# Optimization experiments

Measured on AMD Instinct MI355X. Metric: run time of the kernel, lower is better.

Reference implementation:

```python
import jax, jax.numpy as jnp
from jax import lax
import numpy as np

HID = 32

def setup_inputs() -> dict:
    key = jax.random.key(0)
    ks = jax.random.split(key, 8)
    B, T = 4096, 1024
    x = jax.random.normal(ks[0], (B, T, 1), dtype=jnp.float32)
    h = jnp.zeros((1, B, HID), dtype=jnp.float32)
    s = 1.0 / np.sqrt(HID)  # PyTorch GRU init scale
    W_ih = jax.random.uniform(ks[1], (3 * HID, 1), minval=-s, maxval=s, dtype=jnp.float32)
    W_hh = jax.random.uniform(ks[2], (3 * HID, HID), minval=-s, maxval=s, dtype=jnp.float32)
    b_ih = jax.random.uniform(ks[3], (3 * HID,), minval=-s, maxval=s, dtype=jnp.float32)
    b_hh = jax.random.uniform(ks[4], (3 * HID,), minval=-s, maxval=s, dtype=jnp.float32)
    W_out = jax.random.uniform(ks[5], (1, HID), minval=-s, maxval=s, dtype=jnp.float32)
    b_out = jax.random.uniform(ks[6], (1,), minval=-s, maxval=s, dtype=jnp.float32)
    return {"x": x, "h": h, "W_ih": W_ih, "W_hh": W_hh, "b_ih": b_ih,
            "b_hh": b_hh, "W_out": W_out, "b_out": b_out}

def _gru(x, h0, W_ih, W_hh, b_ih, b_hh):
    # Precompute input projections for all timesteps: [B, T, 3H]
    xi = jnp.einsum('bti,gi->btg', x, W_ih) + b_ih

    def step(h, xi_t):
        gh = h @ W_hh.T + b_hh                      # [B, 3H]
        ir, iz, inn = jnp.split(xi_t, 3, axis=-1)
        hr, hz, hn = jnp.split(gh, 3, axis=-1)
        r = jax.nn.sigmoid(ir + hr)
        z = jax.nn.sigmoid(iz + hz)
        n = jnp.tanh(inn + r * hn)
        h_new = (1.0 - z) * n + z * h               # PyTorch GRU update
        return h_new, h_new

    h_last, hs = lax.scan(step, h0, jnp.swapaxes(xi, 0, 1))  # time-major scan
    return jnp.swapaxes(hs, 0, 1), h_last            # [B,T,H], [B,H]

def reference(x, h, W_ih, W_hh, b_ih, b_hh, W_out, b_out):
    h0 = h[0]                                        # [B, H]
    seq, h_last = _gru(x, h0, W_ih, W_hh, b_ih, b_hh)
    out = jnp.einsum('bth,oh->bto', seq, W_out) + b_out  # [B, T, 1]
    return out, h_last[None]                         # h: [1, B, H]
```

## Files before the change

kernel.cpp:

```cpp
#include <hip/hip_runtime.h>
#include <hip/hip_bf16.h>

#define BATCH 4096
#define T_LEN 1024
#define HID 32
#define CT 64
#define NCHUNK (T_LEN / CT)
#define L2E 1.4426950408889634f

typedef short bf16x8 __attribute__((ext_vector_type(8)));
typedef float f32x4 __attribute__((ext_vector_type(4)));

__device__ __forceinline__ short bf16hi_rne(float f, float* back) {
    unsigned u = __float_as_uint(f);
    unsigned r = (u + 0x7fffu + ((u >> 16) & 1u)) & 0xffff0000u;
    *back = __uint_as_float(r);
    return (short)(r >> 16);
}
__device__ __forceinline__ float fast_rcp(float x)  { return __builtin_amdgcn_rcpf(x); }
__device__ __forceinline__ float fast_exp2(float x) { return __builtin_amdgcn_exp2f(x); }

__global__ void __launch_bounds__(128, 1)
gru_fused3(const float* __restrict__ xg, const float* __restrict__ h0g,
           const float* __restrict__ Wih, const float* __restrict__ Whh,
           const float* __restrict__ bih, const float* __restrict__ bhh,
           const float* __restrict__ Wout, const float* __restrict__ boutp,
           float* __restrict__ outp)
{
    const int tid = threadIdx.x;
    const int w   = tid >> 6;
    const int l   = tid & 63;
    const int rg  = (l >> 4) & 3;
    const int cl  = l & 15;
    const int b0  = blockIdx.x << 4;

    __shared__ float xbuf[16][68];
    __shared__ float po[8][16][68];
    __shared__ __align__(16) short exch[2][2][64 * 8];

    bf16x8 WAhi[3], WAlo[3];
#pragma unroll
    for (int q = 0; q < 3; ++q) {
        const int m = 2 * q + w;
        const float sc = (q < 2) ? L2E : 2.0f * L2E;
#pragma unroll
        for (int i = 0; i < 8; ++i) {
            int j = 16 * ((i >> 2) ^ w) + 4 * rg + (i & 3);
            float wv = Whh[(m * 16 + cl) * HID + j] * sc;
            float hf, d;
            WAhi[q][i] = bf16hi_rne(wv, &hf);
            WAlo[q][i] = bf16hi_rne(wv - hf, &d);
        }
    }
    float wrz[8], brz[8], win[4], bin[4], wout4[4];
    f32x4 biasN;
#pragma unroll
    for (int q = 0; q < 2; ++q)
#pragma unroll
        for (int r = 0; r < 4; ++r) {
            int g = (2 * q + w) * 16 + 4 * rg + r;
            wrz[q * 4 + r] = L2E * Wih[g];
            brz[q * 4 + r] = L2E * (bih[g] + bhh[g]);
        }
#pragma unroll
    for (int r = 0; r < 4; ++r) {
        int g = (4 + w) * 16 + 4 * rg + r;
        win[r]   = 2.0f * L2E * Wih[g];
        bin[r]   = 2.0f * L2E * bih[g];
        biasN[r] = 2.0f * L2E * bhh[g];
        wout4[r] = Wout[16 * w + 4 * rg + r];
    }
    const float bout = boutp[0];

    float h[4];
    bf16x8 Bhi, Blo;
#pragma unroll
    for (int i = 0; i < 8; ++i) {
        int j = 16 * ((i >> 2) ^ w) + 4 * rg + (i & 3);
        float hv = h0g[(size_t)(b0 + cl) * HID + j];
        float hf, d;
        Bhi[i] = bf16hi_rne(hv, &hf);
        Blo[i] = bf16hi_rne(hv - hf, &d);
    }
#pragma unroll
    for (int r = 0; r < 4; ++r)
        h[r] = h0g[(size_t)(b0 + cl) * HID + 16 * w + 4 * rg + r];

    short* const exMy       = &exch[0][w][l * 8];
    const short* const exOt = &exch[0][1 - w][l * 8];

    for (int tc = 0; tc < NCHUNK; ++tc) {
        if (tc > 0) {
            int row = tid >> 3, t0 = (tid & 7) * 8;
            f32x4 s0 = {bout, bout, bout, bout}, s1 = s0;
#pragma unroll
            for (int g = 0; g < 8; ++g) {
                s0 += *reinterpret_cast<const f32x4*>(&po[g][row][t0]);
                s1 += *reinterpret_cast<const f32x4*>(&po[g][row][t0 + 4]);
            }
            float* dst = &outp[(size_t)(b0 + row) * T_LEN + (tc - 1) * CT + t0];
            *reinterpret_cast<f32x4*>(dst)     = s0;
            *reinterpret_cast<f32x4*>(dst + 4) = s1;
        }
#pragma unroll
        for (int q = 0; q < 8; ++q)
            xbuf[w * 8 + q][l] = xg[(size_t)(b0 + w * 8 + q) * T_LEN + tc * CT + l];
        __syncthreads();
        f32x4 xq = *reinterpret_cast<const f32x4*>(&xbuf[cl][0]);

        for (int qt = 0; qt < 16; ++qt) {
            f32x4 xqn = *reinterpret_cast<const f32x4*>(&xbuf[cl][((qt + 1) & 15) * 4]);
            f32x4 opv;
#pragma unroll
            for (int s = 0; s < 4; ++s) {
                const float xv = xq[s];
                f32x4 i0, i1;
#pragma unroll
                for (int r = 0; r < 4; ++r) {
                    i0[r] = fmaf(xv, wrz[r],     brz[r]);
                    i1[r] = fmaf(xv, wrz[4 + r], brz[4 + r]);
                }
                f32x4 a0 = __builtin_amdgcn_mfma_f32_16x16x32_bf16(WAhi[0], Bhi, i0,    0, 0, 0);
                f32x4 a1 = __builtin_amdgcn_mfma_f32_16x16x32_bf16(WAhi[1], Bhi, i1,    0, 0, 0);
                f32x4 a2 = __builtin_amdgcn_mfma_f32_16x16x32_bf16(WAhi[2], Bhi, biasN, 0, 0, 0);
                a0 = __builtin_amdgcn_mfma_f32_16x16x32_bf16(WAhi[0], Blo, a0, 0, 0, 0);
                a1 = __builtin_amdgcn_mfma_f32_16x16x32_bf16(WAhi[1], Blo, a1, 0, 0, 0);
                a2 = __builtin_amdgcn_mfma_f32_16x16x32_bf16(WAhi[2], Blo, a2, 0, 0, 0);
                a0 = __builtin_amdgcn_mfma_f32_16x16x32_bf16(WAlo[0], Bhi, a0, 0, 0, 0);
                a1 = __builtin_amdgcn_mfma_f32_16x16x32_bf16(WAlo[1], Bhi, a1, 0, 0, 0);
                a2 = __builtin_amdgcn_mfma_f32_16x16x32_bf16(WAlo[2], Bhi, a2, 0, 0, 0);

                bf16x8 pk;
                float op = 0.f;
#pragma unroll
                for (int r = 0; r < 4; ++r) {
                    float rr = fast_rcp(1.f + fast_exp2(-a0[r]));
                    float zz = fast_rcp(1.f + fast_exp2(-a1[r]));
                    float np = fmaf(rr, a2[r], fmaf(xv, win[r], bin[r]));
                    float nn = fmaf(-2.f, fast_rcp(1.f + fast_exp2(np)), 1.f);
                    float hv = fmaf(zz, h[r] - nn, nn);
                    h[r] = hv;
                    op = fmaf(hv, wout4[r], op);
                    float hf;
                    pk[r]     = bf16hi_rne(hv, &hf);
                    pk[4 + r] = (short)(__float_as_uint(hv - hf) >> 16);
                }
                opv[s] = op;
                *reinterpret_cast<bf16x8*>(exMy + (s & 1) * 1024) = pk;
                if (s == 3)
                    *reinterpret_cast<f32x4*>(&po[w * 4 + rg][cl][qt * 4]) = opv;
                __syncthreads();
                bf16x8 oth = *reinterpret_cast<const bf16x8*>(exOt + (s & 1) * 1024);
#pragma unroll
                for (int r = 0; r < 4; ++r) {
                    Bhi[r]     = pk[r];      Blo[r]     = pk[4 + r];
                    Bhi[4 + r] = oth[r];     Blo[4 + r] = oth[4 + r];
                }
            }
            xq = xqn;
        }
    }

    {
        int row = tid >> 3, t0 = (tid & 7) * 8;
        f32x4 s0 = {bout, bout, bout, bout}, s1 = s0;
#pragma unroll
        for (int g = 0; g < 8; ++g) {
            s0 += *reinterpret_cast<const f32x4*>(&po[g][row][t0]);
            s1 += *reinterpret_cast<const f32x4*>(&po[g][row][t0 + 4]);
        }
        float* dst = &outp[(size_t)(b0 + row) * T_LEN + (NCHUNK - 1) * CT + t0];
        *reinterpret_cast<f32x4*>(dst)     = s0;
        *reinterpret_cast<f32x4*>(dst + 4) = s1;
    }

#pragma unroll
    for (int r = 0; r < 4; ++r)
        outp[(size_t)BATCH * T_LEN + (size_t)(b0 + cl) * HID + 16 * w + 4 * rg + r] = h[r];
}

extern "C" void kernel_launch(void* const* d_in, const int* in_sizes, int n_in,
                              void* d_out, int out_size, void* d_ws, size_t ws_size,
                              hipStream_t stream) {
    const float* x     = (const float*)d_in[0];
    const float* h0    = (const float*)d_in[1];
    const float* Wih   = (const float*)d_in[2];
    const float* Whh   = (const float*)d_in[3];
    const float* bihv  = (const float*)d_in[4];
    const float* bhhv  = (const float*)d_in[5];
    const float* Woutv = (const float*)d_in[6];
    const float* boutv = (const float*)d_in[7];
    float* out = (float*)d_out;

    gru_fused3<<<dim3(BATCH / 16), dim3(128), 0, stream>>>(
        x, h0, Wih, Whh, bihv, bhhv, Woutv, boutv, out);
}
```

Baseline: 460.1 us.

## Split recurrent MFMA into own-half and exchanged-half products to overlap LDS exchange

```diff
diff --git a/kernel.cpp b/kernel.cpp
--- a/kernel.cpp
+++ b/kernel.cpp
@@ -20,8 +20,10 @@
 __device__ __forceinline__ float fast_rcp(float x)  { return __builtin_amdgcn_rcpf(x); }
 __device__ __forceinline__ float fast_exp2(float x) { return __builtin_amdgcn_exp2f(x); }
 
+#define MFMA __builtin_amdgcn_mfma_f32_16x16x32_bf16
+
 __global__ void __launch_bounds__(128, 1)
-gru_fused3(const float* __restrict__ xg, const float* __restrict__ h0g,
+gru_fused5(const float* __restrict__ xg, const float* __restrict__ h0g,
            const float* __restrict__ Wih, const float* __restrict__ Whh,
            const float* __restrict__ bih, const float* __restrict__ bhh,
            const float* __restrict__ Wout, const float* __restrict__ boutp,
@@ -38,22 +40,29 @@
     __shared__ float po[8][16][68];
     __shared__ __align__(16) short exch[2][2][64 * 8];
 
-    bf16x8 WAhi[3], WAlo[3];
+    bf16x8 AownHi[3], AownLo[3], AothHi[3], AothLo[3];
 #pragma unroll
     for (int q = 0; q < 3; ++q) {
         const int m = 2 * q + w;
         const float sc = (q < 2) ? L2E : 2.0f * L2E;
 #pragma unroll
         for (int i = 0; i < 8; ++i) {
-            int j = 16 * ((i >> 2) ^ w) + 4 * rg + (i & 3);
-            float wv = Whh[(m * 16 + cl) * HID + j] * sc;
-            float hf, d;
-            WAhi[q][i] = bf16hi_rne(wv, &hf);
-            WAlo[q][i] = bf16hi_rne(wv - hf, &d);
+            if (i < 4) {
+                float hf, d;
+                float wv = Whh[(m * 16 + cl) * HID + 16 * w + 4 * rg + i] * sc;
+                AownHi[q][i] = bf16hi_rne(wv, &hf);
+                AownLo[q][i] = bf16hi_rne(wv - hf, &d);
+                float wv2 = Whh[(m * 16 + cl) * HID + 16 * (1 - w) + 4 * rg + i] * sc;
+                AothHi[q][i] = bf16hi_rne(wv2, &hf);
+                AothLo[q][i] = bf16hi_rne(wv2 - hf, &d);
+            } else {
+                AownHi[q][i] = 0; AownLo[q][i] = 0;
+                AothHi[q][i] = 0; AothLo[q][i] = 0;
+            }
         }
     }
     float wrz[8], brz[8], win[4], bin[4], wout4[4];
-    f32x4 biasN;
+    f32x4 bN;
 #pragma unroll
     for (int q = 0; q < 2; ++q)
 #pragma unroll
@@ -67,24 +76,24 @@
         int g = (4 + w) * 16 + 4 * rg + r;
         win[r]   = 2.0f * L2E * Wih[g];
         bin[r]   = 2.0f * L2E * bih[g];
-        biasN[r] = 2.0f * L2E * bhh[g];
+        bN[r]    = 2.0f * L2E * bhh[g];
         wout4[r] = Wout[16 * w + 4 * rg + r];
     }
     const float bout = boutp[0];
 
     float h[4];
-    bf16x8 Bhi, Blo;
-#pragma unroll
-    for (int i = 0; i < 8; ++i) {
-        int j = 16 * ((i >> 2) ^ w) + 4 * rg + (i & 3);
-        float hv = h0g[(size_t)(b0 + cl) * HID + j];
-        float hf, d;
-        Bhi[i] = bf16hi_rne(hv, &hf);
-        Blo[i] = bf16hi_rne(hv - hf, &d);
-    }
-#pragma unroll
-    for (int r = 0; r < 4; ++r)
-        h[r] = h0g[(size_t)(b0 + cl) * HID + 16 * w + 4 * rg + r];
+    bf16x8 pk, R;
+#pragma unroll
+    for (int r = 0; r < 4; ++r) {
+        float hv = h0g[(size_t)(b0 + cl) * HID + 16 * w + 4 * rg + r];
+        h[r] = hv;
+        float hf;
+        pk[r]     = bf16hi_rne(hv, &hf);
+        pk[4 + r] = (short)(__float_as_uint(hv - hf) >> 16);
+        float ov = h0g[(size_t)(b0 + cl) * HID + 16 * (1 - w) + 4 * rg + r];
+        R[r]     = bf16hi_rne(ov, &hf);
+        R[4 + r] = (short)(__float_as_uint(ov - hf) >> 16);
+    }
 
     short* const exMy       = &exch[0][w][l * 8];
     const short* const exOt = &exch[0][1 - w][l * 8];
@@ -114,48 +123,56 @@
 #pragma unroll
             for (int s = 0; s < 4; ++s) {
                 const float xv = xq[s];
-                f32x4 i0, i1;
+                bf16x8 pkLo = __builtin_shufflevector(pk, pk, 4, 5, 6, 7, 0, 1, 2, 3);
+                bf16x8 RLo  = __builtin_shufflevector(R,  R,  4, 5, 6, 7, 0, 1, 2, 3);
+                f32x4 iR, iZ;
 #pragma unroll
                 for (int r = 0; r < 4; ++r) {
-                    i0[r] = fmaf(xv, wrz[r],     brz[r]);
-                    i1[r] = fmaf(xv, wrz[4 + r], brz[4 + r]);
+                    iR[r] = fmaf(xv, wrz[r],     brz[r]);
+                    iZ[r] = fmaf(xv, wrz[4 + r], brz[4 + r]);
                 }
-                f32x4 a0 = __builtin_amdgcn_mfma_f32_16x16x32_bf16(WAhi[0], Bhi, i0,    0, 0, 0);
-                f32x4 a1 = __builtin_amdgcn_mfma_f32_16x16x32_bf16(WAhi[1], Bhi, i1,    0, 0, 0);
-                f32x4 a2 = __builtin_amdgcn_mfma_f32_16x16x32_bf16(WAhi[2], Bhi, biasN, 0, 0, 0);
-                a0 = __builtin_amdgcn_mfma_f32_16x16x32_bf16(WAhi[0], Blo, a0, 0, 0, 0);
-                a1 = __builtin_amdgcn_mfma_f32_16x16x32_bf16(WAhi[1], Blo, a1, 0, 0, 0);
-                a2 = __builtin_amdgcn_mfma_f32_16x16x32_bf16(WAhi[2], Blo, a2, 0, 0, 0);
-                a0 = __builtin_amdgcn_mfma_f32_16x16x32_bf16(WAlo[0], Bhi, a0, 0, 0, 0);
-                a1 = __builtin_amdgcn_mfma_f32_16x16x32_bf16(WAlo[1], Bhi, a1, 0, 0, 0);
-                a2 = __builtin_amdgcn_mfma_f32_16x16x32_bf16(WAlo[2], Bhi, a2, 0, 0, 0);
-
-                bf16x8 pk;
+                f32x4 aR, aZ, aN;
+                aR = MFMA(AownHi[0], pk,   iR, 0, 0, 0);
+                aZ = MFMA(AownHi[1], pk,   iZ, 0, 0, 0);
+                aN = MFMA(AownHi[2], pk,   bN, 0, 0, 0);
+                aR = MFMA(AownLo[0], pk,   aR, 0, 0, 0);
+                aZ = MFMA(AownLo[1], pk,   aZ, 0, 0, 0);
+                aN = MFMA(AownLo[2], pk,   aN, 0, 0, 0);
+                aR = MFMA(AownHi[0], pkLo, aR, 0, 0, 0);
+                aZ = MFMA(AownHi[1], pkLo, aZ, 0, 0, 0);
+                aN = MFMA(AownHi[2], pkLo, aN, 0, 0, 0);
+                aR = MFMA(AothHi[0], R,    aR, 0, 0, 0);
+                aZ = MFMA(AothHi[1], R,    aZ, 0, 0, 0);
+                aN = MFMA(AothHi[2], R,    aN, 0, 0, 0);
+                aR = MFMA(AothLo[0], R,    aR, 0, 0, 0);
+                aZ = MFMA(AothLo[1], R,    aZ, 0, 0, 0);
+                aN = MFMA(AothLo[2], R,    aN, 0, 0, 0);
+                aR = MFMA(AothHi[0], RLo,  aR, 0, 0, 0);
+                aZ = MFMA(AothHi[1], RLo,  aZ, 0, 0, 0);
+                aN = MFMA(AothHi[2], RLo,  aN, 0, 0, 0);
+
+                bf16x8 npk;
                 float op = 0.f;
 #pragma unroll
                 for (int r = 0; r < 4; ++r) {
-                    float rr = fast_rcp(1.f + fast_exp2(-a0[r]));
-                    float zz = fast_rcp(1.f + fast_exp2(-a1[r]));
-                    float np = fmaf(rr, a2[r], fmaf(xv, win[r], bin[r]));
+                    float rr = fast_rcp(1.f + fast_exp2(-aR[r]));
+                    float zz = fast_rcp(1.f + fast_exp2(-aZ[r]));
+                    float np = fmaf(rr, aN[r], fmaf(xv, win[r], bin[r]));
                     float nn = fmaf(-2.f, fast_rcp(1.f + fast_exp2(np)), 1.f);
                     float hv = fmaf(zz, h[r] - nn, nn);
                     h[r] = hv;
                     op = fmaf(hv, wout4[r], op);
                     float hf;
-                    pk[r]     = bf16hi_rne(hv, &hf);
-                    pk[4 + r] = (short)(__float_as_uint(hv - hf) >> 16);
+                    npk[r]     = bf16hi_rne(hv, &hf);
+                    npk[4 + r] = (short)(__float_as_uint(hv - hf) >> 16);
                 }
+                pk = npk;
                 opv[s] = op;
                 *reinterpret_cast<bf16x8*>(exMy + (s & 1) * 1024) = pk;
                 if (s == 3)
                     *reinterpret_cast<f32x4*>(&po[w * 4 + rg][cl][qt * 4]) = opv;
                 __syncthreads();
-                bf16x8 oth = *reinterpret_cast<const bf16x8*>(exOt + (s & 1) * 1024);
-#pragma unroll
-                for (int r = 0; r < 4; ++r) {
-                    Bhi[r]     = pk[r];      Blo[r]     = pk[4 + r];
-                    Bhi[4 + r] = oth[r];     Blo[4 + r] = oth[4 + r];
-                }
+                R = *reinterpret_cast<const bf16x8*>(exOt + (s & 1) * 1024);
             }
             xq = xqn;
         }
@@ -192,6 +209,6 @@
     const float* boutv = (const float*)d_in[7];
     float* out = (float*)d_out;
 
-    gru_fused3<<<dim3(BATCH / 16), dim3(128), 0, stream>>>(
+    gru_fused5<<<dim3(BATCH / 16), dim3(128), 0, stream>>>(
         x, h0, Wih, Whh, bihv, bhhv, Woutv, boutv, out);
 }
```

Result: slower. 491.5 us (+6.8%).

## Split GRU hidden units across four waves with duplicated-A bf16 split MFMA layout

Applied to the files above, without the earlier changes.

```diff
diff --git a/kernel.cpp b/kernel.cpp
--- a/kernel.cpp
+++ b/kernel.cpp
@@ -9,6 +9,7 @@
 #define L2E 1.4426950408889634f
 
 typedef short bf16x8 __attribute__((ext_vector_type(8)));
+typedef short short4v __attribute__((ext_vector_type(4)));
 typedef float f32x4 __attribute__((ext_vector_type(4)));
 
 __device__ __forceinline__ short bf16hi_rne(float f, float* back) {
@@ -20,91 +21,110 @@
 __device__ __forceinline__ float fast_rcp(float x)  { return __builtin_amdgcn_rcpf(x); }
 __device__ __forceinline__ float fast_exp2(float x) { return __builtin_amdgcn_exp2f(x); }
 
-__global__ void __launch_bounds__(128, 1)
-gru_fused3(const float* __restrict__ xg, const float* __restrict__ h0g,
+#define MFMA __builtin_amdgcn_mfma_f32_16x16x32_bf16
+
+__global__ void __launch_bounds__(256, 1)
+gru_fused6(const float* __restrict__ xg, const float* __restrict__ h0g,
            const float* __restrict__ Wih, const float* __restrict__ Whh,
            const float* __restrict__ bih, const float* __restrict__ bhh,
            const float* __restrict__ Wout, const float* __restrict__ boutp,
            float* __restrict__ outp)
 {
-    const int tid = threadIdx.x;
-    const int w   = tid >> 6;
-    const int l   = tid & 63;
-    const int rg  = (l >> 4) & 3;
-    const int cl  = l & 15;
-    const int b0  = blockIdx.x << 4;
+    const int tid  = threadIdx.x;
+    const int v    = tid >> 6;
+    const int half = v & 1;
+    const int sub  = v >> 1;
+    const int l    = tid & 63;
+    const int rg   = (l >> 4) & 3;
+    const int cl   = l & 15;
+    const int b0   = blockIdx.x << 4;
 
     __shared__ float xbuf[16][68];
-    __shared__ float po[8][16][68];
-    __shared__ __align__(16) short exch[2][2][64 * 8];
-
-    bf16x8 WAhi[3], WAlo[3];
+    __shared__ float po[16][16][68];
+    __shared__ __align__(16) short ex[2][2][4][16][8];
+    const int PAR = 2 * 4 * 16 * 8;
+
+    bf16x8 A1[3][2], A2[3][2];
+    const int phicl = 4 * (cl >> 2) + 2 * sub + (cl & 1);
 #pragma unroll
     for (int q = 0; q < 3; ++q) {
-        const int m = 2 * q + w;
+        const int m = 2 * q + half;
         const float sc = (q < 2) ? L2E : 2.0f * L2E;
-#pragma unroll
-        for (int i = 0; i < 8; ++i) {
-            int j = 16 * ((i >> 2) ^ w) + 4 * rg + (i & 3);
-            float wv = Whh[(m * 16 + cl) * HID + j] * sc;
-            float hf, d;
-            WAhi[q][i] = bf16hi_rne(wv, &hf);
-            WAlo[q][i] = bf16hi_rne(wv - hf, &d);
-        }
-    }
-    float wrz[8], brz[8], win[4], bin[4], wout4[4];
-    f32x4 biasN;
-#pragma unroll
-    for (int q = 0; q < 2; ++q)
-#pragma unroll
-        for (int r = 0; r < 4; ++r) {
-            int g = (2 * q + w) * 16 + 4 * rg + r;
-            wrz[q * 4 + r] = L2E * Wih[g];
-            brz[q * 4 + r] = L2E * (bih[g] + bhh[g]);
-        }
-#pragma unroll
-    for (int r = 0; r < 4; ++r) {
-        int g = (4 + w) * 16 + 4 * rg + r;
-        win[r]   = 2.0f * L2E * Wih[g];
-        bin[r]   = 2.0f * L2E * bih[g];
-        biasN[r] = 2.0f * L2E * bhh[g];
-        wout4[r] = Wout[16 * w + 4 * rg + r];
+        const int grow = m * 16 + phicl;
+#pragma unroll
+        for (int kh = 0; kh < 2; ++kh)
+#pragma unroll
+            for (int qs = 0; qs < 4; ++qs) {
+                float wv = Whh[grow * HID + 16 * kh + 4 * rg + qs] * sc;
+                float hf, d;
+                short hi = bf16hi_rne(wv, &hf);
+                short lo = bf16hi_rne(wv - hf, &d);
+                int shi = (qs < 2) ? qs : qs + 2;
+                int slo = (qs < 2) ? qs + 2 : qs + 4;
+                A1[q][kh][shi] = hi;  A1[q][kh][slo] = hi;
+                A2[q][kh][shi] = lo;  A2[q][kh][slo] = 0;
+            }
+    }
+    float wr4[4], br4[4], wz4[4], bz4[4], wn2[2], bn2[2], wo2[2];
+    f32x4 bN;
+#pragma unroll
+    for (int u = 0; u < 4; ++u) {
+        int rrow = 4 * rg + 2 * sub + (u & 1);
+        int gr = half * 16 + rrow;
+        int gz = (2 + half) * 16 + rrow;
+        int gn = (4 + half) * 16 + rrow;
+        wr4[u] = L2E * Wih[gr];  br4[u] = L2E * (bih[gr] + bhh[gr]);
+        wz4[u] = L2E * Wih[gz];  bz4[u] = L2E * (bih[gz] + bhh[gz]);
+        bN[u]  = 2.0f * L2E * bhh[gn];
+    }
+#pragma unroll
+    for (int u = 0; u < 2; ++u) {
+        int rrow = 4 * rg + 2 * sub + u;
+        int gn = (4 + half) * 16 + rrow;
+        wn2[u] = 2.0f * L2E * Wih[gn];
+        bn2[u] = 2.0f * L2E * bih[gn];
+        wo2[u] = Wout[half * 16 + rrow];
     }
     const float bout = boutp[0];
 
-    float h[4];
-    bf16x8 Bhi, Blo;
-#pragma unroll
-    for (int i = 0; i < 8; ++i) {
-        int j = 16 * ((i >> 2) ^ w) + 4 * rg + (i & 3);
-        float hv = h0g[(size_t)(b0 + cl) * HID + j];
-        float hf, d;
-        Bhi[i] = bf16hi_rne(hv, &hf);
-        Blo[i] = bf16hi_rne(hv - hf, &d);
-    }
-#pragma unroll
-    for (int r = 0; r < 4; ++r)
-        h[r] = h0g[(size_t)(b0 + cl) * HID + 16 * w + 4 * rg + r];
-
-    short* const exMy       = &exch[0][w][l * 8];
-    const short* const exOt = &exch[0][1 - w][l * 8];
+    float h2[2];
+#pragma unroll
+    for (int u = 0; u < 2; ++u)
+        h2[u] = h0g[(size_t)(b0 + cl) * HID + 16 * half + 4 * rg + 2 * sub + u];
+    bf16x8 B0, B1;
+#pragma unroll
+    for (int qs = 0; qs < 4; ++qs) {
+        int shi = (qs < 2) ? qs : qs + 2;
+        int slo = (qs < 2) ? qs + 2 : qs + 4;
+        float hv0 = h0g[(size_t)(b0 + cl) * HID + 4 * rg + qs];
+        float hf;
+        B0[shi] = bf16hi_rne(hv0, &hf);
+        B0[slo] = (short)(__float_as_uint(hv0 - hf) >> 16);
+        float hv1 = h0g[(size_t)(b0 + cl) * HID + 16 + 4 * rg + qs];
+        B1[shi] = bf16hi_rne(hv1, &hf);
+        B1[slo] = (short)(__float_as_uint(hv1 - hf) >> 16);
+    }
+
+    short* const exW        = &ex[0][half][rg][cl][sub * 4];
+    const short* const exR0 = &ex[0][0][rg][cl][0];
+    const short* const exR1 = &ex[0][1][rg][cl][0];
 
     for (int tc = 0; tc < NCHUNK; ++tc) {
         if (tc > 0) {
-            int row = tid >> 3, t0 = (tid & 7) * 8;
-            f32x4 s0 = {bout, bout, bout, bout}, s1 = s0;
-#pragma unroll
-            for (int g = 0; g < 8; ++g) {
-                s0 += *reinterpret_cast<const f32x4*>(&po[g][row][t0]);
-                s1 += *reinterpret_cast<const f32x4*>(&po[g][row][t0 + 4]);
-            }
-            float* dst = &outp[(size_t)(b0 + row) * T_LEN + (tc - 1) * CT + t0];
-            *reinterpret_cast<f32x4*>(dst)     = s0;
-            *reinterpret_cast<f32x4*>(dst + 4) = s1;
+            int row = tid >> 4, seg = tid & 15;
+            f32x4 sacc = {bout, bout, bout, bout};
+#pragma unroll
+            for (int g = 0; g < 16; ++g)
+                sacc += *reinterpret_cast<const f32x4*>(&po[g][row][seg * 4]);
+            *reinterpret_cast<f32x4*>(
+                &outp[(size_t)(b0 + row) * T_LEN + (tc - 1) * CT + seg * 4]) = sacc;
         }
-#pragma unroll
-        for (int q = 0; q < 8; ++q)
-            xbuf[w * 8 + q][l] = xg[(size_t)(b0 + w * 8 + q) * T_LEN + tc * CT + l];
+        {
+            int row = tid >> 4, seg = tid & 15;
+            *reinterpret_cast<f32x4*>(&xbuf[row][seg * 4]) =
+                *reinterpret_cast<const f32x4*>(
+                    &xg[(size_t)(b0 + row) * T_LEN + tc * CT + seg * 4]);
+        }
         __syncthreads();
         f32x4 xq = *reinterpret_cast<const f32x4*>(&xbuf[cl][0]);
 
@@ -114,69 +134,67 @@
 #pragma unroll
             for (int s = 0; s < 4; ++s) {
                 const float xv = xq[s];
-                f32x4 i0, i1;
-#pragma unroll
-                for (int r = 0; r < 4; ++r) {
-                    i0[r] = fmaf(xv, wrz[r],     brz[r]);
-                    i1[r] = fmaf(xv, wrz[4 + r], brz[4 + r]);
+                f32x4 iR, iZ;
+#pragma unroll
+                for (int u = 0; u < 4; ++u) {
+                    iR[u] = fmaf(xv, wr4[u], br4[u]);
+                    iZ[u] = fmaf(xv, wz4[u], bz4[u]);
                 }
-                f32x4 a0 = __builtin_amdgcn_mfma_f32_16x16x32_bf16(WAhi[0], Bhi, i0,    0, 0, 0);
-                f32x4 a1 = __builtin_amdgcn_mfma_f32_16x16x32_bf16(WAhi[1], Bhi, i1,    0, 0, 0);
-                f32x4 a2 = __builtin_amdgcn_mfma_f32_16x16x32_bf16(WAhi[2], Bhi, biasN, 0, 0, 0);
-                a0 = __builtin_amdgcn_mfma_f32_16x16x32_bf16(WAhi[0], Blo, a0, 0, 0, 0);
-                a1 = __builtin_amdgcn_mfma_f32_16x16x32_bf16(WAhi[1], Blo, a1, 0, 0, 0);
-                a2 = __builtin_amdgcn_mfma_f32_16x16x32_bf16(WAhi[2], Blo, a2, 0, 0, 0);
-                a0 = __builtin_amdgcn_mfma_f32_16x16x32_bf16(WAlo[0], Bhi, a0, 0, 0, 0);
-                a1 = __builtin_amdgcn_mfma_f32_16x16x32_bf16(WAlo[1], Bhi, a1, 0, 0, 0);
-                a2 = __builtin_amdgcn_mfma_f32_16x16x32_bf16(WAlo[2], Bhi, a2, 0, 0, 0);
-
-                bf16x8 pk;
+                f32x4 aR, aZ, aN;
+                aR = MFMA(A1[0][0], B0, iR, 0, 0, 0);
+                aZ = MFMA(A1[1][0], B0, iZ, 0, 0, 0);
+                aN = MFMA(A1[2][0], B0, bN, 0, 0, 0);
+                aR = MFMA(A2[0][0], B0, aR, 0, 0, 0);
+                aZ = MFMA(A2[1][0], B0, aZ, 0, 0, 0);
+                aN = MFMA(A2[2][0], B0, aN, 0, 0, 0);
+                aR = MFMA(A1[0][1], B1, aR, 0, 0, 0);
+                aZ = MFMA(A1[1][1], B1, aZ, 0, 0, 0);
+                aN = MFMA(A1[2][1], B1, aN, 0, 0, 0);
+                aR = MFMA(A2[0][1], B1, aR, 0, 0, 0);
+                aZ = MFMA(A2[1][1], B1, aZ, 0, 0, 0);
+                aN = MFMA(A2[2][1], B1, aN, 0, 0, 0);
+
                 float op = 0.f;
-#pragma unroll
-                for (int r = 0; r < 4; ++r) {
-                    float rr = fast_rcp(1.f + fast_exp2(-a0[r]));
-                    float zz = fast_rcp(1.f + fast_exp2(-a1[r]));
-                    float np = fmaf(rr, a2[r], fmaf(xv, win[r], bin[r]));
+                short4v pkv;
+#pragma unroll
+                for (int u = 0; u < 2; ++u) {
+                    float rr = fast_rcp(1.f + fast_exp2(-aR[u]));
+                    float zz = fast_rcp(1.f + fast_exp2(-aZ[u]));
+                    float np = fmaf(rr, aN[u], fmaf(xv, wn2[u], bn2[u]));
                     float nn = fmaf(-2.f, fast_rcp(1.f + fast_exp2(np)), 1.f);
-                    float hv = fmaf(zz, h[r] - nn, nn);
-                    h[r] = hv;
-                    op = fmaf(hv, wout4[r], op);
+                    float hv = fmaf(zz, h2[u] - nn, nn);
+                    h2[u] = hv;
+                    op = fmaf(hv, wo2[u], op);
                     float hf;
-                    pk[r]     = bf16hi_rne(hv, &hf);
-                    pk[4 + r] = (short)(__float_as_uint(hv - hf) >> 16);
+                    pkv[u]     = bf16hi_rne(hv, &hf);
+                    pkv[2 + u] = (short)(__float_as_uint(hv - hf) >> 16);
                 }
                 opv[s] = op;
-                *reinterpret_cast<bf16x8*>(exMy + (s & 1) * 1024) = pk;
+                *reinterpret_cast<short4v*>(exW + (s & 1) * PAR) = pkv;
                 if (s == 3)
-                    *reinterpret_cast<f32x4*>(&po[w * 4 + rg][cl][qt * 4]) = opv;
+                    *reinterpret_cast<f32x4*>(&po[v * 4 + rg][cl][qt * 4]) = opv;
                 __syncthreads();
-                bf16x8 oth = *reinterpret_cast<const bf16x8*>(exOt + (s & 1) * 1024);
-#pragma unroll
-                for (int r = 0; r < 4; ++r) {
-                    Bhi[r]     = pk[r];      Blo[r]     = pk[4 + r];
-                    Bhi[4 + r] = oth[r];     Blo[4 + r] = oth[4 + r];
-                }
+                B0 = *reinterpret_cast<const bf16x8*>(exR0 + (s & 1) * PAR);
+                B1 = *reinterpret_cast<const bf16x8*>(exR1 + (s & 1) * PAR);
             }
             xq = xqn;
         }
     }
 
     {
-        int row = tid >> 3, t0 = (tid & 7) * 8;
-        f32x4 s0 = {bout, bout, bout, bout}, s1 = s0;
-#pragma unroll
-        for (int g = 0; g < 8; ++g) {
-            s0 += *reinterpret_cast<const f32x4*>(&po[g][row][t0]);
-            s1 += *reinterpret_cast<const f32x4*>(&po[g][row][t0 + 4]);
-        }
-        float* dst = &outp[(size_t)(b0 + row) * T_LEN + (NCHUNK - 1) * CT + t0];
-        *reinterpret_cast<f32x4*>(dst)     = s0;
-        *reinterpret_cast<f32x4*>(dst + 4) = s1;
-    }
-
-#pragma unroll
-    for (int r = 0; r < 4; ++r)
-        outp[(size_t)BATCH * T_LEN + (size_t)(b0 + cl) * HID + 16 * w + 4 * rg + r] = h[r];
+        int row = tid >> 4, seg = tid & 15;
+        f32x4 sacc = {bout, bout, bout, bout};
+#pragma unroll
+        for (int g = 0; g < 16; ++g)
+            sacc += *reinterpret_cast<const f32x4*>(&po[g][row][seg * 4]);
+        *reinterpret_cast<f32x4*>(
+            &outp[(size_t)(b0 + row) * T_LEN + (NCHUNK - 1) * CT + seg * 4]) = sacc;
+    }
+
+#pragma unroll
+    for (int u = 0; u < 2; ++u)
+        outp[(size_t)BATCH * T_LEN + (size_t)(b0 + cl) * HID
+             + 16 * half + 4 * rg + 2 * sub + u] = h2[u];
 }
 
 extern "C" void kernel_launch(void* const* d_in, const int* in_sizes, int n_in,
@@ -192,6 +210,6 @@
     const float* boutv = (const float*)d_in[7];
     float* out = (float*)d_out;
 
-    gru_fused3<<<dim3(BATCH / 16), dim3(128), 0, stream>>>(
+    gru_fused6<<<dim3(BATCH / 16), dim3(256), 0, stream>>>(
         x, h0, Wih, Whh, bihv, bhhv, Woutv, boutv, out);
 }
```

Measured after the change: 400.3 us. 1.15x faster.
